# Kernel optimization log

Hardware: AMD Instinct MI355X
Metric: run time of the kernel (lower is better)

Reference implementation:

```python
import jax, jax.numpy as jnp
import numpy as np

N_NODES = 50000
N_EDGES = 400000
NODE_F = 128
EDGE_F = 64
HID = 128
N_LAYERS = 2


def _mlp(x, w1, b1, w2, b2):
    # Linear -> ReLU -> Linear
    return jnp.maximum(x @ w1 + b1, 0.0) @ w2 + b2


def setup_inputs() -> dict:
    key = jax.random.key(0)
    ks = jax.random.split(key, 24)
    s = 0.02
    inp = {
        "node_features": jax.random.normal(ks[0], (N_NODES, NODE_F), jnp.float32),
        "edge_list": jax.random.randint(ks[1], (N_EDGES, 2), 0, N_NODES, jnp.int32),
        "edge_features": jax.random.normal(ks[2], (N_EDGES, EDGE_F), jnp.float32),
        "num_nodes": N_NODES,
        # node encoder
        "ne_w1": jax.random.normal(ks[3], (NODE_F, HID), jnp.float32) * s,
        "ne_b1": jnp.zeros((HID,), jnp.float32),
        "ne_w2": jax.random.normal(ks[4], (HID, HID), jnp.float32) * s,
        "ne_b2": jnp.zeros((HID,), jnp.float32),
        # edge encoder
        "ee_w1": jax.random.normal(ks[5], (EDGE_F, HID), jnp.float32) * s,
        "ee_b1": jnp.zeros((HID,), jnp.float32),
        "ee_w2": jax.random.normal(ks[6], (HID, HID), jnp.float32) * s,
        "ee_b2": jnp.zeros((HID,), jnp.float32),
        # message layers (stacked over num_layers)
        "ml_w1": jax.random.normal(ks[7], (N_LAYERS, 3 * HID, HID), jnp.float32) * s,
        "ml_b1": jnp.zeros((N_LAYERS, HID), jnp.float32),
        "ml_w2": jax.random.normal(ks[8], (N_LAYERS, HID, HID), jnp.float32) * s,
        "ml_b2": jnp.zeros((N_LAYERS, HID), jnp.float32),
        # aggregation
        "agg_w1": jax.random.normal(ks[9], (HID, HID), jnp.float32) * s,
        "agg_b1": jnp.zeros((HID,), jnp.float32),
        "agg_w2": jax.random.normal(ks[10], (HID, HID), jnp.float32) * s,
        "agg_b2": jnp.zeros((HID,), jnp.float32),
    }
    return inp


def reference(node_features, edge_list, edge_features, num_nodes,
              ne_w1, ne_b1, ne_w2, ne_b2,
              ee_w1, ee_b1, ee_w2, ee_b2,
              ml_w1, ml_b1, ml_w2, ml_b2,
              agg_w1, agg_b1, agg_w2, agg_b2):
    node_emb = _mlp(node_features, ne_w1, ne_b1, ne_w2, ne_b2)   # [N, H]
    edge_emb = _mlp(edge_features, ee_w1, ee_b1, ee_w2, ee_b2)   # [E, H]
    src = edge_list[:, 0]
    dst = edge_list[:, 1]
    for l in range(ml_w1.shape[0]):
        h_s = node_emb[src]                                      # [E, H] gather
        h_d = node_emb[dst]                                      # [E, H] gather
        # message src->dst and dst->src (the torch loop does both directions)
        m_fwd = _mlp(jnp.concatenate([h_s, edge_emb, h_d], axis=-1),
                     ml_w1[l], ml_b1[l], ml_w2[l], ml_b2[l])     # [E, H]
        m_bwd = _mlp(jnp.concatenate([h_d, edge_emb, h_s], axis=-1),
                     ml_w1[l], ml_b1[l], ml_w2[l], ml_b2[l])     # [E, H]
        new_node_emb = node_emb.at[dst].add(m_fwd).at[src].add(m_bwd)
        node_emb = _mlp(new_node_emb, agg_w1, agg_b1, agg_w2, agg_b2)
    return node_emb
```

## Files before the change

### kernel.cpp

```cpp
#include <hip/hip_runtime.h>

typedef float fx4 __attribute__((ext_vector_type(4)));
typedef float f32x4 __attribute__((ext_vector_type(4)));
typedef unsigned short us4v __attribute__((ext_vector_type(4)));
typedef unsigned short us8 __attribute__((ext_vector_type(8)));
typedef __bf16 bf8 __attribute__((ext_vector_type(8)));

static __device__ __forceinline__ fx4 ld4(const float* p) {
    return *reinterpret_cast<const fx4*>(p);
}
static __device__ __forceinline__ void st4(float* p, fx4 v) {
    *reinterpret_cast<fx4*>(p) = v;
}
static __device__ __forceinline__ unsigned short f2bf(float f) {
    union { float f; unsigned int i; } x; x.f = f;
    unsigned int r = x.i + 0x7FFF + ((x.i >> 16) & 1);
    return (unsigned short)(r >> 16);
}
static __device__ __forceinline__ float bf2f(unsigned int u) {
    union { unsigned int i; float f; } x; x.i = u << 16; return x.f;
}
static __device__ __forceinline__ us4v pk4(f32x4 v) {
    us4v u;
    #pragma unroll
    for (int j = 0; j < 4; ++j) u[j] = f2bf(v[j]);
    return u;
}

static __device__ __forceinline__ f32x4 mfma16(us8 a, us8 b, f32x4 c) {
    return __builtin_amdgcn_mfma_f32_16x16x32_bf16(
        __builtin_bit_cast(bf8, a), __builtin_bit_cast(bf8, b), c, 0, 0, 0);
}

template <int K1, bool AF32, bool BIAS, bool RELU, bool OUTF, bool OUTB, bool XMODE>
__global__ __launch_bounds__(256) void mfma_gemm(
    const void* __restrict__ Av, const unsigned short* __restrict__ Wt,
    const float* __restrict__ bias,
    float* __restrict__ outF, unsigned short* __restrict__ outB,
    const float* __restrict__ resid, const int* __restrict__ startp, int M)
{
    constexpr int KP = K1 + 8;
    __shared__ unsigned short Ws[128 * KP];
    const int tid = threadIdx.x;
    const int lane = tid & 63;
    const int wv = tid >> 6;
    const int row0 = blockIdx.x * 128 + wv * 32;

    constexpr int C8 = K1 / 8;
    for (int i = tid; i < 128 * C8; i += 256) {
        int r = i / C8, c = (i % C8) * 8;
        *reinterpret_cast<us8*>(&Ws[r * KP + c]) =
            *reinterpret_cast<const us8*>(&Wt[r * K1 + c]);
    }
    __syncthreads();

    const int ar = lane & 15;
    const int ak = (lane >> 4) * 8;

    f32x4 acc[2][8];
    #pragma unroll
    for (int m = 0; m < 2; ++m)
        #pragma unroll
        for (int nt = 0; nt < 8; ++nt) acc[m][nt] = {0.f, 0.f, 0.f, 0.f};

    #pragma unroll
    for (int kk = 0; kk < K1 / 32; ++kk) {
        us8 a[2];
        #pragma unroll
        for (int m = 0; m < 2; ++m) {
            int row = row0 + m * 16 + ar;
            us8 t = 0;
            if (row < M) {
                if (AF32) {
                    const float* ap = (const float*)Av + (size_t)row * K1 + kk * 32 + ak;
                    fx4 x0 = ld4(ap), x1 = ld4(ap + 4);
                    #pragma unroll
                    for (int j = 0; j < 4; ++j) {
                        t[j] = f2bf(x0[j]);
                        t[4 + j] = f2bf(x1[j]);
                    }
                } else {
                    t = *reinterpret_cast<const us8*>(
                        (const unsigned short*)Av + (size_t)row * K1 + kk * 32 + ak);
                }
            }
            a[m] = t;
        }
        #pragma unroll
        for (int nt = 0; nt < 8; ++nt) {
            us8 b = *reinterpret_cast<const us8*>(&Ws[(nt * 16 + ar) * KP + kk * 32 + ak]);
            acc[0][nt] = mfma16(b, a[0], acc[0][nt]);
            acc[1][nt] = mfma16(b, a[1], acc[1][nt]);
        }
    }

    const int q = lane >> 4;
    #pragma unroll
    for (int m = 0; m < 2; ++m) {
        int r = row0 + m * 16 + (lane & 15);
        if (r >= M) continue;
        float deg = 0.f;
        if (XMODE) deg = (float)(startp[r + 1] - startp[r]);
        #pragma unroll
        for (int nt = 0; nt < 8; ++nt) {
            int c0 = nt * 16 + q * 4;
            f32x4 o = acc[m][nt];
            if (XMODE) {
                fx4 bb = ld4(bias + c0);
                fx4 rr = ld4(resid + (size_t)r * 128 + c0);
                #pragma unroll
                for (int j = 0; j < 4; ++j) o[j] += rr[j] + deg * bb[j];
            } else if (BIAS) {
                fx4 bb = ld4(bias + c0);
                #pragma unroll
                for (int j = 0; j < 4; ++j) o[j] += bb[j];
            }
            if (RELU) {
                #pragma unroll
                for (int j = 0; j < 4; ++j) o[j] = fmaxf(o[j], 0.f);
            }
            if (OUTF) st4(outF + (size_t)r * 128 + c0, o);
            if (OUTB) *reinterpret_cast<us4v*>(&outB[(size_t)r * 128 + c0]) = pk4(o);
        }
    }
}

template <bool AF32, bool OUTF, bool OUTB>
__global__ __launch_bounds__(256) void mfma_mlp(
    const void* __restrict__ Av, const unsigned short* __restrict__ W1t,
    const float* __restrict__ b1, const unsigned short* __restrict__ W2t,
    const float* __restrict__ b2,
    float* __restrict__ outF, unsigned short* __restrict__ outB, int M)
{
    constexpr int KP = 136;
    __shared__ unsigned short Ws1[128 * KP];
    __shared__ unsigned short Ws2[128 * KP];
    const int tid = threadIdx.x;
    const int lane = tid & 63;
    const int wv = tid >> 6;
    const int row0 = blockIdx.x * 128 + wv * 32;

    for (int i = tid; i < 128 * 16; i += 256) {
        int r = i >> 4, c = (i & 15) * 8;
        *reinterpret_cast<us8*>(&Ws1[r * KP + c]) =
            *reinterpret_cast<const us8*>(&W1t[r * 128 + c]);
        *reinterpret_cast<us8*>(&Ws2[r * KP + c]) =
            *reinterpret_cast<const us8*>(&W2t[r * 128 + c]);
    }
    __syncthreads();

    const int ar = lane & 15;
    const int ak = (lane >> 4) * 8;
    const int q = lane >> 4;

    f32x4 acc[2][8];
    #pragma unroll
    for (int m = 0; m < 2; ++m)
        #pragma unroll
        for (int nt = 0; nt < 8; ++nt) acc[m][nt] = {0.f, 0.f, 0.f, 0.f};

    #pragma unroll
    for (int kk = 0; kk < 4; ++kk) {
        us8 a[2];
        #pragma unroll
        for (int m = 0; m < 2; ++m) {
            int row = row0 + m * 16 + ar;
            us8 t = 0;
            if (row < M) {
                if (AF32) {
                    const float* ap = (const float*)Av + (size_t)row * 128 + kk * 32 + ak;
                    fx4 x0 = ld4(ap), x1 = ld4(ap + 4);
                    #pragma unroll
                    for (int j = 0; j < 4; ++j) {
                        t[j] = f2bf(x0[j]);
                        t[4 + j] = f2bf(x1[j]);
                    }
                } else {
                    t = *reinterpret_cast<const us8*>(
                        (const unsigned short*)Av + (size_t)row * 128 + kk * 32 + ak);
                }
            }
            a[m] = t;
        }
        #pragma unroll
        for (int nt = 0; nt < 8; ++nt) {
            us8 b = *reinterpret_cast<const us8*>(&Ws1[(nt * 16 + ar) * KP + kk * 32 + ak]);
            acc[0][nt] = mfma16(b, a[0], acc[0][nt]);
            acc[1][nt] = mfma16(b, a[1], acc[1][nt]);
        }
    }
    __syncthreads();

    #pragma unroll
    for (int m = 0; m < 2; ++m) {
        int lrow = wv * 32 + m * 16 + (lane & 15);
        #pragma unroll
        for (int nt = 0; nt < 8; ++nt) {
            int c0 = nt * 16 + q * 4;
            fx4 bb = ld4(b1 + c0);
            f32x4 o = acc[m][nt];
            #pragma unroll
            for (int j = 0; j < 4; ++j) o[j] = fmaxf(o[j] + bb[j], 0.f);
            *reinterpret_cast<us4v*>(&Ws1[lrow * KP + c0]) = pk4(o);
        }
    }
    __syncthreads();

    f32x4 acc2[2][8];
    #pragma unroll
    for (int m = 0; m < 2; ++m)
        #pragma unroll
        for (int nt = 0; nt < 8; ++nt) acc2[m][nt] = {0.f, 0.f, 0.f, 0.f};

    #pragma unroll
    for (int kk = 0; kk < 4; ++kk) {
        us8 a[2];
        #pragma unroll
        for (int m = 0; m < 2; ++m) {
            int lrow = wv * 32 + m * 16 + ar;
            a[m] = *reinterpret_cast<const us8*>(&Ws1[lrow * KP + kk * 32 + ak]);
        }
        #pragma unroll
        for (int nt = 0; nt < 8; ++nt) {
            us8 b = *reinterpret_cast<const us8*>(&Ws2[(nt * 16 + ar) * KP + kk * 32 + ak]);
            acc2[0][nt] = mfma16(b, a[0], acc2[0][nt]);
            acc2[1][nt] = mfma16(b, a[1], acc2[1][nt]);
        }
    }

    #pragma unroll
    for (int m = 0; m < 2; ++m) {
        int r = row0 + m * 16 + (lane & 15);
        if (r >= M) continue;
        #pragma unroll
        for (int nt = 0; nt < 8; ++nt) {
            int c0 = nt * 16 + q * 4;
            fx4 bb = ld4(b2 + c0);
            f32x4 o = acc2[m][nt];
            #pragma unroll
            for (int j = 0; j < 4; ++j) o[j] += bb[j];
            if (OUTF) st4(outF + (size_t)r * 128 + c0, o);
            if (OUTB) *reinterpret_cast<us4v*>(&outB[(size_t)r * 128 + c0]) = pk4(o);
        }
    }
}

__global__ __launch_bounds__(256) void mfma_gemm_dual(
    const float* __restrict__ A, const unsigned short* __restrict__ Wt,
    unsigned short* __restrict__ out1, unsigned short* __restrict__ out2, int M)
{
    constexpr int KP = 136;
    __shared__ unsigned short Ws[256 * KP];
    const int tid = threadIdx.x;
    const int lane = tid & 63;
    const int wv = tid >> 6;
    const int row0 = blockIdx.x * 128 + wv * 32;

    for (int i = tid; i < 256 * 16; i += 256) {
        int r = i >> 4, c = (i & 15) * 8;
        *reinterpret_cast<us8*>(&Ws[r * KP + c]) =
            *reinterpret_cast<const us8*>(&Wt[r * 128 + c]);
    }
    __syncthreads();

    const int ar = lane & 15;
    const int ak = (lane >> 4) * 8;
    const int q = lane >> 4;

    f32x4 acc[2][16];
    #pragma unroll
    for (int m = 0; m < 2; ++m)
        #pragma unroll
        for (int nt = 0; nt < 16; ++nt) acc[m][nt] = {0.f, 0.f, 0.f, 0.f};

    #pragma unroll
    for (int kk = 0; kk < 4; ++kk) {
        us8 a[2];
        #pragma unroll
        for (int m = 0; m < 2; ++m) {
            int row = row0 + m * 16 + ar;
            us8 t = 0;
            if (row < M) {
                const float* ap = A + (size_t)row * 128 + kk * 32 + ak;
                fx4 x0 = ld4(ap), x1 = ld4(ap + 4);
                #pragma unroll
                for (int j = 0; j < 4; ++j) {
                    t[j] = f2bf(x0[j]);
                    t[4 + j] = f2bf(x1[j]);
                }
            }
            a[m] = t;
        }
        #pragma unroll
        for (int nt = 0; nt < 16; ++nt) {
            us8 b = *reinterpret_cast<const us8*>(&Ws[(nt * 16 + ar) * KP + kk * 32 + ak]);
            acc[0][nt] = mfma16(b, a[0], acc[0][nt]);
            acc[1][nt] = mfma16(b, a[1], acc[1][nt]);
        }
    }

    #pragma unroll
    for (int m = 0; m < 2; ++m) {
        int r = row0 + m * 16 + (lane & 15);
        if (r >= M) continue;
        #pragma unroll
        for (int nt = 0; nt < 16; ++nt) {
            int c0 = (nt & 7) * 16 + q * 4;
            unsigned short* o = (nt < 8) ? out1 : out2;
            *reinterpret_cast<us4v*>(&o[(size_t)r * 128 + c0]) = pk4(acc[m][nt]);
        }
    }
}

__global__ __launch_bounds__(256) void gemm128_kernel(
    const float* __restrict__ X, const float* __restrict__ W,
    float* __restrict__ Out, int M)
{
    __shared__ float Xs[64 * 132];
    const int tid = threadIdx.x;
    const int row0 = blockIdx.x * 64;

    for (int i = tid; i < 64 * 32; i += 256) {
        int r = i >> 5, c = (i & 31) * 4;
        fx4 v = {0.f, 0.f, 0.f, 0.f};
        int gr = row0 + r;
        if (gr < M) v = ld4(X + (size_t)gr * 128 + c);
        st4(&Xs[r * 132 + c], v);
    }
    __syncthreads();

    const int ty = tid >> 4, tx = tid & 15;
    fx4 acc[4][2];
    #pragma unroll
    for (int r = 0; r < 4; ++r) { acc[r][0] = 0.f; acc[r][1] = 0.f; }
    for (int k = 0; k < 128; k += 4) {
        fx4 xr[4];
        #pragma unroll
        for (int r = 0; r < 4; ++r) xr[r] = ld4(&Xs[(ty * 4 + r) * 132 + k]);
        #pragma unroll
        for (int kk = 0; kk < 4; ++kk) {
            fx4 wa = ld4(W + (size_t)(k + kk) * 128 + tx * 8);
            fx4 wb = ld4(W + (size_t)(k + kk) * 128 + tx * 8 + 4);
            #pragma unroll
            for (int r = 0; r < 4; ++r) {
                acc[r][0] += xr[r][kk] * wa;
                acc[r][1] += xr[r][kk] * wb;
            }
        }
    }
    #pragma unroll
    for (int r = 0; r < 4; ++r) {
        int gr = row0 + ty * 4 + r;
        if (gr < M) {
            st4(Out + (size_t)gr * 128 + tx * 8, acc[r][0]);
            st4(Out + (size_t)gr * 128 + tx * 8 + 4, acc[r][1]);
        }
    }
}

struct TJob { const float* src; unsigned short* dst; int K; };
struct TJobs { TJob j[16]; };

__global__ __launch_bounds__(256) void transpose_kernel(TJobs jobs) {
    TJob t = jobs.j[blockIdx.x];
    int total = 128 * t.K;
    for (int i = threadIdx.x; i < total; i += 256) {
        int n = i / t.K, k = i - n * t.K;
        t.dst[(size_t)n * t.K + k] = f2bf(t.src[(size_t)k * 128 + n]);
    }
}

__global__ __launch_bounds__(128) void bep_kernel(
    const float* __restrict__ ee_b2, const float* __restrict__ ml_w1,
    const float* __restrict__ ml_b1, float* __restrict__ bep)
{
    int l = blockIdx.x, n = threadIdx.x;
    const float* W1b = ml_w1 + (size_t)l * 384 * 128 + 128 * 128;
    float s = ml_b1[(size_t)l * 128 + n];
    for (int k = 0; k < 128; ++k) s += ee_b2[k] * W1b[(size_t)k * 128 + n];
    bep[(size_t)l * 128 + n] = s;
}

__global__ __launch_bounds__(256) void csr_hist_kernel(
    const int* __restrict__ el, int* __restrict__ cnt, int NE)
{
    int e = blockIdx.x * 256 + threadIdx.x;
    if (e < NE) {
        atomicAdd(&cnt[el[2 * (size_t)e + 1]], 1);
        atomicAdd(&cnt[el[2 * (size_t)e]], 1);
    }
}

__global__ __launch_bounds__(256) void scan_p1_kernel(
    const int* __restrict__ cnt, int* __restrict__ bsum, int NN)
{
    __shared__ int red[256];
    const int t = threadIdx.x;
    int i = blockIdx.x * 256 + t;
    red[t] = (i < NN) ? cnt[i] : 0;
    __syncthreads();
    for (int off = 128; off > 0; off >>= 1) {
        if (t < off) red[t] += red[t + off];
        __syncthreads();
    }
    if (t == 0) bsum[blockIdx.x] = red[0];
}

__global__ __launch_bounds__(256) void scan_p2_kernel(
    int* __restrict__ bsum, int* __restrict__ startp, int nb, int NN)
{
    __shared__ int part[256];
    const int t = threadIdx.x;
    int v = (t < nb) ? bsum[t] : 0;
    part[t] = v;
    __syncthreads();
    for (int off = 1; off < 256; off <<= 1) {
        int u = (t >= off) ? part[t - off] : 0;
        __syncthreads();
        part[t] += u;
        __syncthreads();
    }
    if (t < nb) bsum[t] = part[t] - v;
    if (t == 255) startp[NN] = part[255];
}

__global__ __launch_bounds__(256) void scan_p3_kernel(
    int* __restrict__ cnt, const int* __restrict__ bsum,
    int* __restrict__ startp, int NN)
{
    __shared__ int part[256];
    const int t = threadIdx.x;
    int i = blockIdx.x * 256 + t;
    int v = (i < NN) ? cnt[i] : 0;
    part[t] = v;
    __syncthreads();
    for (int off = 1; off < 256; off <<= 1) {
        int u = (t >= off) ? part[t - off] : 0;
        __syncthreads();
        part[t] += u;
        __syncthreads();
    }
    if (i < NN) {
        startp[i] = bsum[blockIdx.x] + part[t] - v;
        cnt[i] = 0;
    }
}

__global__ __launch_bounds__(256) void csr_fill_kernel(
    const int* __restrict__ el, const int* __restrict__ startp,
    int* __restrict__ cursor, int2* __restrict__ inc, int NE)
{
    int e = blockIdx.x * 256 + threadIdx.x;
    if (e < NE) {
        int s = el[2 * (size_t)e], d = el[2 * (size_t)e + 1];
        int p = startp[d] + atomicAdd(&cursor[d], 1);
        inc[p] = make_int2(s, e);
        int q = startp[s] + atomicAdd(&cursor[s], 1);
        inc[q] = make_int2(d, e);
    }
}

__global__ __launch_bounds__(256) void gather_kernel(
    const unsigned short* __restrict__ P1bf, const unsigned short* __restrict__ P3bf,
    const unsigned short* __restrict__ Ep, const int2* __restrict__ inc,
    const int* __restrict__ startp, unsigned short* __restrict__ S, int M)
{
    const int tid = threadIdx.x;
    const int lane = tid & 63;
    const int n = blockIdx.x * 4 + (tid >> 6);
    if (n >= M) return;
    const int slot = lane >> 4;
    const int c = (lane & 15) * 8;

    float p3[8], acc[8];
    us8 u3 = *reinterpret_cast<const us8*>(&P3bf[(size_t)n * 128 + c]);
    #pragma unroll
    for (int i = 0; i < 8; ++i) {
        p3[i] = bf2f((unsigned int)(unsigned short)u3[i]);
        acc[i] = 0.f;
    }

    const int j1 = startp[n + 1];
    int j = startp[n] + slot;
    int2 oe = (j < j1) ? inc[j] : make_int2(0, 0);
    while (j < j1) {
        int jn = j + 4;
        int2 oen = (jn < j1) ? inc[jn] : make_int2(0, 0);
        us8 u1 = *reinterpret_cast<const us8*>(&P1bf[(size_t)oe.x * 128 + c]);
        us8 ue = *reinterpret_cast<const us8*>(&Ep[(size_t)oe.y * 128 + c]);
        #pragma unroll
        for (int i = 0; i < 8; ++i)
            acc[i] += fmaxf(p3[i] + bf2f((unsigned int)(unsigned short)u1[i])
                                  + bf2f((unsigned int)(unsigned short)ue[i]), 0.f);
        j = jn; oe = oen;
    }

    #pragma unroll
    for (int i = 0; i < 8; ++i) {
        acc[i] += __shfl_xor(acc[i], 16, 64);
        acc[i] += __shfl_xor(acc[i], 32, 64);
    }
    if (slot == 0) {
        us8 pk;
        #pragma unroll
        for (int i = 0; i < 8; ++i) pk[i] = f2bf(acc[i]);
        *reinterpret_cast<us8*>(&S[(size_t)n * 128 + c]) = pk;
    }
}

extern "C" void kernel_launch(void* const* d_in, const int* in_sizes, int n_in,
                              void* d_out, int out_size, void* d_ws, size_t ws_size,
                              hipStream_t stream) {
    const float* node_f    = (const float*)d_in[0];
    const int*   edge_list = (const int*)d_in[1];
    const float* edge_f    = (const float*)d_in[2];
    const float* ne_w1 = (const float*)d_in[4];
    const float* ne_b1 = (const float*)d_in[5];
    const float* ne_w2 = (const float*)d_in[6];
    const float* ne_b2 = (const float*)d_in[7];
    const float* ee_w1 = (const float*)d_in[8];
    const float* ee_b1 = (const float*)d_in[9];
    const float* ee_w2 = (const float*)d_in[10];
    const float* ee_b2 = (const float*)d_in[11];
    const float* ml_w1 = (const float*)d_in[12];
    const float* ml_b1 = (const float*)d_in[13];
    const float* ml_w2 = (const float*)d_in[14];
    const float* ml_b2 = (const float*)d_in[15];
    const float* agg_w1 = (const float*)d_in[16];
    const float* agg_b1 = (const float*)d_in[17];
    const float* agg_w2 = (const float*)d_in[18];
    const float* agg_b2 = (const float*)d_in[19];

    const int NN = in_sizes[0] / 128;
    const int NE = in_sizes[1] / 2;
    const int n_layers = in_sizes[12] / (384 * 128);

    char* p = (char*)d_ws;
    auto alloc = [&](size_t bytes) -> void* {
        void* r = (void*)p;
        p += (bytes + 255) & ~(size_t)255;
        return r;
    };
    float* node_emb = (float*)alloc((size_t)NN * 128 * 4);
    unsigned short* P1bf = (unsigned short*)alloc((size_t)NN * 128 * 2);
    unsigned short* P3bf = (unsigned short*)alloc((size_t)NN * 128 * 2);
    unsigned short* bufS = (unsigned short*)alloc((size_t)NN * 128 * 2);
    unsigned short* H_edge = (unsigned short*)alloc((size_t)NE * 128 * 2);
    unsigned short* Ep = (unsigned short*)alloc((size_t)NE * 128 * 2);
    unsigned short* ne_w1t = (unsigned short*)alloc(128 * 128 * 2);
    unsigned short* ne_w2t = (unsigned short*)alloc(128 * 128 * 2);
    unsigned short* ee_w1t = (unsigned short*)alloc(128 * 64 * 2);
    unsigned short* aw1t = (unsigned short*)alloc(128 * 128 * 2);
    unsigned short* aw2t = (unsigned short*)alloc(128 * 128 * 2);
    unsigned short* W13t[2], *W2t[2], *Wept[2];
    float* Wepf[2];
    for (int l = 0; l < 2; ++l) {
        W13t[l] = (unsigned short*)alloc(256 * 128 * 2);
        W2t[l]  = (unsigned short*)alloc(128 * 128 * 2);
        Wept[l] = (unsigned short*)alloc(128 * 128 * 2);
        Wepf[l] = (float*)alloc(128 * 128 * 4);
    }
    float* bep = (float*)alloc((size_t)2 * 128 * 4);
    int* cnt = (int*)alloc((size_t)NN * 4);
    int* startp = (int*)alloc((size_t)(NN + 1) * 4);
    int* bsum = (int*)alloc(256 * 4);
    int2* inc = (int2*)alloc((size_t)2 * NE * 8);
    size_t need = (size_t)(p - (char*)d_ws);
    if (ws_size < need) return;

    dim3 blk(256);
    const int gM_N = (NN + 127) / 128;
    const int gM_E = (NE + 127) / 128;
    const int gE256 = (NE + 255) / 256;
    const int nbScan = (NN + 255) / 256;

    for (int l = 0; l < n_layers && l < 2; ++l) {
        const float* W1b = ml_w1 + (size_t)l * 384 * 128 + 128 * 128;
        gemm128_kernel<<<2, blk, 0, stream>>>(ee_w2, W1b, Wepf[l], 128);
    }
    {
        TJobs jobs{};
        int nj = 0;
        jobs.j[nj++] = {ne_w1, ne_w1t, 128};
        jobs.j[nj++] = {ne_w2, ne_w2t, 128};
        jobs.j[nj++] = {ee_w1, ee_w1t, 64};
        jobs.j[nj++] = {agg_w1, aw1t, 128};
        jobs.j[nj++] = {agg_w2, aw2t, 128};
        for (int l = 0; l < n_layers && l < 2; ++l) {
            jobs.j[nj++] = {ml_w1 + (size_t)l * 384 * 128, W13t[l], 128};
            jobs.j[nj++] = {ml_w1 + (size_t)l * 384 * 128 + 256 * 128, W13t[l] + 128 * 128, 128};
            jobs.j[nj++] = {ml_w2 + (size_t)l * 128 * 128, W2t[l], 128};
            jobs.j[nj++] = {Wepf[l], Wept[l], 128};
        }
        transpose_kernel<<<nj, blk, 0, stream>>>(jobs);
    }
    bep_kernel<<<n_layers, 128, 0, stream>>>(ee_b2, ml_w1, ml_b1, bep);

    mfma_mlp<true, true, false><<<gM_N, blk, 0, stream>>>(
        node_f, ne_w1t, ne_b1, ne_w2t, ne_b2, node_emb, nullptr, NN);
    mfma_gemm<64, true, true, true, false, true, false><<<gM_E, blk, 0, stream>>>(
        edge_f, ee_w1t, ee_b1, nullptr, H_edge, nullptr, nullptr, NE);

    hipMemsetAsync(cnt, 0, (size_t)NN * sizeof(int), stream);
    csr_hist_kernel<<<gE256, blk, 0, stream>>>(edge_list, cnt, NE);
    scan_p1_kernel<<<nbScan, blk, 0, stream>>>(cnt, bsum, NN);
    scan_p2_kernel<<<1, blk, 0, stream>>>(bsum, startp, nbScan, NN);
    scan_p3_kernel<<<nbScan, blk, 0, stream>>>(cnt, bsum, startp, NN);
    csr_fill_kernel<<<gE256, blk, 0, stream>>>(edge_list, startp, cnt, inc, NE);

    float* out = (float*)d_out;
    for (int l = 0; l < n_layers && l < 2; ++l) {
        mfma_gemm_dual<<<gM_N, blk, 0, stream>>>(node_emb, W13t[l], P1bf, P3bf, NN);
        mfma_gemm<128, false, true, false, false, true, false><<<gM_E, blk, 0, stream>>>(
            H_edge, Wept[l], bep + (size_t)l * 128, nullptr, Ep, nullptr, nullptr, NE);
        gather_kernel<<<(NN + 3) / 4, blk, 0, stream>>>(
            P1bf, P3bf, Ep, inc, startp, bufS, NN);
        mfma_gemm<128, false, true, false, false, true, true><<<gM_N, blk, 0, stream>>>(
            bufS, W2t[l], ml_b2 + (size_t)l * 128, nullptr, P1bf, node_emb, startp, NN);
        float* dst = (l == n_layers - 1) ? out : node_emb;
        mfma_mlp<false, true, false><<<gM_N, blk, 0, stream>>>(
            P1bf, aw1t, agg_b1, aw2t, agg_b2, dst, nullptr, NN);
    }
}
```

Measured before the change: 588.0 us.

## Fuse edge encoder with per-layer edge projections and read weights from global

Adds an edge_mega kernel that computes the edge encoder hidden layer into LDS and then directly produces both layers' projected edge terms. This removes the H_edge intermediate round trip and the per-layer edge GEMM launches. The GEMM and MLP kernels also stop staging weights in LDS and load B fragments straight from global or L2, which cuts LDS use and the startup sync but adds repeated global loads. The dual node GEMM is split into two single GEMMs, which reads node_emb twice.

```diff
diff --git a/kernel.cpp b/kernel.cpp
--- a/kernel.cpp
+++ b/kernel.cpp
@@ -30,6 +30,29 @@
 static __device__ __forceinline__ f32x4 mfma16(us8 a, us8 b, f32x4 c) {
     return __builtin_amdgcn_mfma_f32_16x16x32_bf16(
         __builtin_bit_cast(bf8, a), __builtin_bit_cast(bf8, b), c, 0, 0, 0);
+}
+
+template <int K1, bool AF32>
+static __device__ __forceinline__ void loadA(
+    const void* __restrict__ Av, int row0, int ar, int ak, int kk, int M, us8 a[2])
+{
+    #pragma unroll
+    for (int m = 0; m < 2; ++m) {
+        int row = row0 + m * 16 + ar;
+        us8 t = 0;
+        if (row < M) {
+            if (AF32) {
+                const float* ap = (const float*)Av + (size_t)row * K1 + kk * 32 + ak;
+                fx4 x0 = ld4(ap), x1 = ld4(ap + 4);
+                #pragma unroll
+                for (int j = 0; j < 4; ++j) { t[j] = f2bf(x0[j]); t[4 + j] = f2bf(x1[j]); }
+            } else {
+                t = *reinterpret_cast<const us8*>(
+                    (const unsigned short*)Av + (size_t)row * K1 + kk * 32 + ak);
+            }
+        }
+        a[m] = t;
+    }
 }
 
 template <int K1, bool AF32, bool BIAS, bool RELU, bool OUTF, bool OUTB, bool XMODE>
@@ -39,21 +62,11 @@
     float* __restrict__ outF, unsigned short* __restrict__ outB,
     const float* __restrict__ resid, const int* __restrict__ startp, int M)
 {
-    constexpr int KP = K1 + 8;
-    __shared__ unsigned short Ws[128 * KP];
     const int tid = threadIdx.x;
     const int lane = tid & 63;
     const int wv = tid >> 6;
     const int row0 = blockIdx.x * 128 + wv * 32;
 
-    constexpr int C8 = K1 / 8;
-    for (int i = tid; i < 128 * C8; i += 256) {
-        int r = i / C8, c = (i % C8) * 8;
-        *reinterpret_cast<us8*>(&Ws[r * KP + c]) =
-            *reinterpret_cast<const us8*>(&Wt[r * K1 + c]);
-    }
-    __syncthreads();
-
     const int ar = lane & 15;
     const int ak = (lane >> 4) * 8;
 
@@ -66,31 +79,16 @@
     #pragma unroll
     for (int kk = 0; kk < K1 / 32; ++kk) {
         us8 a[2];
-        #pragma unroll
-        for (int m = 0; m < 2; ++m) {
-            int row = row0 + m * 16 + ar;
-            us8 t = 0;
-            if (row < M) {
-                if (AF32) {
-                    const float* ap = (const float*)Av + (size_t)row * K1 + kk * 32 + ak;
-                    fx4 x0 = ld4(ap), x1 = ld4(ap + 4);
-                    #pragma unroll
-                    for (int j = 0; j < 4; ++j) {
-                        t[j] = f2bf(x0[j]);
-                        t[4 + j] = f2bf(x1[j]);
-                    }
-                } else {
-                    t = *reinterpret_cast<const us8*>(
-                        (const unsigned short*)Av + (size_t)row * K1 + kk * 32 + ak);
-                }
-            }
-            a[m] = t;
-        }
-        #pragma unroll
-        for (int nt = 0; nt < 8; ++nt) {
-            us8 b = *reinterpret_cast<const us8*>(&Ws[(nt * 16 + ar) * KP + kk * 32 + ak]);
-            acc[0][nt] = mfma16(b, a[0], acc[0][nt]);
-            acc[1][nt] = mfma16(b, a[1], acc[1][nt]);
+        loadA<K1, AF32>(Av, row0, ar, ak, kk, M, a);
+        us8 b[8];
+        #pragma unroll
+        for (int nt = 0; nt < 8; ++nt)
+            b[nt] = *reinterpret_cast<const us8*>(
+                &Wt[(size_t)(nt * 16 + ar) * K1 + kk * 32 + ak]);
+        #pragma unroll
+        for (int nt = 0; nt < 8; ++nt) {
+            acc[0][nt] = mfma16(b[nt], a[0], acc[0][nt]);
+            acc[1][nt] = mfma16(b[nt], a[1], acc[1][nt]);
         }
     }
 
@@ -133,22 +131,12 @@
     float* __restrict__ outF, unsigned short* __restrict__ outB, int M)
 {
     constexpr int KP = 136;
-    __shared__ unsigned short Ws1[128 * KP];
-    __shared__ unsigned short Ws2[128 * KP];
+    __shared__ unsigned short Hs[128 * KP];
     const int tid = threadIdx.x;
     const int lane = tid & 63;
     const int wv = tid >> 6;
     const int row0 = blockIdx.x * 128 + wv * 32;
 
-    for (int i = tid; i < 128 * 16; i += 256) {
-        int r = i >> 4, c = (i & 15) * 8;
-        *reinterpret_cast<us8*>(&Ws1[r * KP + c]) =
-            *reinterpret_cast<const us8*>(&W1t[r * 128 + c]);
-        *reinterpret_cast<us8*>(&Ws2[r * KP + c]) =
-            *reinterpret_cast<const us8*>(&W2t[r * 128 + c]);
-    }
-    __syncthreads();
-
     const int ar = lane & 15;
     const int ak = (lane >> 4) * 8;
     const int q = lane >> 4;
@@ -162,34 +150,18 @@
     #pragma unroll
     for (int kk = 0; kk < 4; ++kk) {
         us8 a[2];
-        #pragma unroll
-        for (int m = 0; m < 2; ++m) {
-            int row = row0 + m * 16 + ar;
-            us8 t = 0;
-            if (row < M) {
-                if (AF32) {
-                    const float* ap = (const float*)Av + (size_t)row * 128 + kk * 32 + ak;
-                    fx4 x0 = ld4(ap), x1 = ld4(ap + 4);
-                    #pragma unroll
-                    for (int j = 0; j < 4; ++j) {
-                        t[j] = f2bf(x0[j]);
-                        t[4 + j] = f2bf(x1[j]);
-                    }
-                } else {
-                    t = *reinterpret_cast<const us8*>(
-                        (const unsigned short*)Av + (size_t)row * 128 + kk * 32 + ak);
-                }
-            }
-            a[m] = t;
-        }
-        #pragma unroll
-        for (int nt = 0; nt < 8; ++nt) {
-            us8 b = *reinterpret_cast<const us8*>(&Ws1[(nt * 16 + ar) * KP + kk * 32 + ak]);
-            acc[0][nt] = mfma16(b, a[0], acc[0][nt]);
-            acc[1][nt] = mfma16(b, a[1], acc[1][nt]);
-        }
-    }
-    __syncthreads();
+        loadA<128, AF32>(Av, row0, ar, ak, kk, M, a);
+        us8 b[8];
+        #pragma unroll
+        for (int nt = 0; nt < 8; ++nt)
+            b[nt] = *reinterpret_cast<const us8*>(
+                &W1t[(size_t)(nt * 16 + ar) * 128 + kk * 32 + ak]);
+        #pragma unroll
+        for (int nt = 0; nt < 8; ++nt) {
+            acc[0][nt] = mfma16(b[nt], a[0], acc[0][nt]);
+            acc[1][nt] = mfma16(b[nt], a[1], acc[1][nt]);
+        }
+    }
 
     #pragma unroll
     for (int m = 0; m < 2; ++m) {
@@ -201,7 +173,7 @@
             f32x4 o = acc[m][nt];
             #pragma unroll
             for (int j = 0; j < 4; ++j) o[j] = fmaxf(o[j] + bb[j], 0.f);
-            *reinterpret_cast<us4v*>(&Ws1[lrow * KP + c0]) = pk4(o);
+            *reinterpret_cast<us4v*>(&Hs[lrow * KP + c0]) = pk4(o);
         }
     }
     __syncthreads();
@@ -216,15 +188,18 @@
     for (int kk = 0; kk < 4; ++kk) {
         us8 a[2];
         #pragma unroll
-        for (int m = 0; m < 2; ++m) {
-            int lrow = wv * 32 + m * 16 + ar;
-            a[m] = *reinterpret_cast<const us8*>(&Ws1[lrow * KP + kk * 32 + ak]);
-        }
-        #pragma unroll
-        for (int nt = 0; nt < 8; ++nt) {
-            us8 b = *reinterpret_cast<const us8*>(&Ws2[(nt * 16 + ar) * KP + kk * 32 + ak]);
-            acc2[0][nt] = mfma16(b, a[0], acc2[0][nt]);
-            acc2[1][nt] = mfma16(b, a[1], acc2[1][nt]);
+        for (int m = 0; m < 2; ++m)
+            a[m] = *reinterpret_cast<const us8*>(
+                &Hs[(wv * 32 + m * 16 + ar) * KP + kk * 32 + ak]);
+        us8 b[8];
+        #pragma unroll
+        for (int nt = 0; nt < 8; ++nt)
+            b[nt] = *reinterpret_cast<const us8*>(
+                &W2t[(size_t)(nt * 16 + ar) * 128 + kk * 32 + ak]);
+        #pragma unroll
+        for (int nt = 0; nt < 8; ++nt) {
+            acc2[0][nt] = mfma16(b[nt], a[0], acc2[0][nt]);
+            acc2[1][nt] = mfma16(b[nt], a[1], acc2[1][nt]);
         }
     }
 
@@ -245,69 +220,105 @@
     }
 }
 
-__global__ __launch_bounds__(256) void mfma_gemm_dual(
-    const float* __restrict__ A, const unsigned short* __restrict__ Wt,
-    unsigned short* __restrict__ out1, unsigned short* __restrict__ out2, int M)
+__global__ __launch_bounds__(256) void edge_mega(
+    const float* __restrict__ edge_f, const unsigned short* __restrict__ W1t,
+    const float* __restrict__ b1,
+    const unsigned short* __restrict__ Wep0t, const unsigned short* __restrict__ Wep1t,
+    const float* __restrict__ bep,
+    unsigned short* __restrict__ Ep0, unsigned short* __restrict__ Ep1,
+    int nout, int M)
 {
     constexpr int KP = 136;
-    __shared__ unsigned short Ws[256 * KP];
+    __shared__ unsigned short Hs[128 * KP];
     const int tid = threadIdx.x;
     const int lane = tid & 63;
     const int wv = tid >> 6;
     const int row0 = blockIdx.x * 128 + wv * 32;
 
-    for (int i = tid; i < 256 * 16; i += 256) {
-        int r = i >> 4, c = (i & 15) * 8;
-        *reinterpret_cast<us8*>(&Ws[r * KP + c]) =
-            *reinterpret_cast<const us8*>(&Wt[r * 128 + c]);
-    }
-    __syncthreads();
-
     const int ar = lane & 15;
     const int ak = (lane >> 4) * 8;
     const int q = lane >> 4;
 
-    f32x4 acc[2][16];
+    f32x4 acc[2][8];
     #pragma unroll
     for (int m = 0; m < 2; ++m)
         #pragma unroll
-        for (int nt = 0; nt < 16; ++nt) acc[m][nt] = {0.f, 0.f, 0.f, 0.f};
-
-    #pragma unroll
-    for (int kk = 0; kk < 4; ++kk) {
+        for (int nt = 0; nt < 8; ++nt) acc[m][nt] = {0.f, 0.f, 0.f, 0.f};
+
+    #pragma unroll
+    for (int kk = 0; kk < 2; ++kk) {
         us8 a[2];
+        loadA<64, true>(edge_f, row0, ar, ak, kk, M, a);
+        us8 b[8];
+        #pragma unroll
+        for (int nt = 0; nt < 8; ++nt)
+            b[nt] = *reinterpret_cast<const us8*>(
+                &W1t[(size_t)(nt * 16 + ar) * 64 + kk * 32 + ak]);
+        #pragma unroll
+        for (int nt = 0; nt < 8; ++nt) {
+            acc[0][nt] = mfma16(b[nt], a[0], acc[0][nt]);
+            acc[1][nt] = mfma16(b[nt], a[1], acc[1][nt]);
+        }
+    }
+
+    #pragma unroll
+    for (int m = 0; m < 2; ++m) {
+        int lrow = wv * 32 + m * 16 + (lane & 15);
+        #pragma unroll
+        for (int nt = 0; nt < 8; ++nt) {
+            int c0 = nt * 16 + q * 4;
+            fx4 bb = ld4(b1 + c0);
+            f32x4 o = acc[m][nt];
+            #pragma unroll
+            for (int j = 0; j < 4; ++j) o[j] = fmaxf(o[j] + bb[j], 0.f);
+            *reinterpret_cast<us4v*>(&Hs[lrow * KP + c0]) = pk4(o);
+        }
+    }
+    __syncthreads();
+
+    for (int l = 0; l < nout; ++l) {
+        const unsigned short* Wt = (l == 0) ? Wep0t : Wep1t;
+        unsigned short* Out = (l == 0) ? Ep0 : Ep1;
+        const float* bl = bep + (size_t)l * 128;
+
+        f32x4 acc2[2][8];
+        #pragma unroll
+        for (int m = 0; m < 2; ++m)
+            #pragma unroll
+            for (int nt = 0; nt < 8; ++nt) acc2[m][nt] = {0.f, 0.f, 0.f, 0.f};
+
+        #pragma unroll
+        for (int kk = 0; kk < 4; ++kk) {
+            us8 a[2];
+            #pragma unroll
+            for (int m = 0; m < 2; ++m)
+                a[m] = *reinterpret_cast<const us8*>(
+                    &Hs[(wv * 32 + m * 16 + ar) * KP + kk * 32 + ak]);
+            us8 b[8];
+            #pragma unroll
+            for (int nt = 0; nt < 8; ++nt)
+                b[nt] = *reinterpret_cast<const us8*>(
+                    &Wt[(size_t)(nt * 16 + ar) * 128 + kk * 32 + ak]);
+            #pragma unroll
+            for (int nt = 0; nt < 8; ++nt) {
+                acc2[0][nt] = mfma16(b[nt], a[0], acc2[0][nt]);
+                acc2[1][nt] = mfma16(b[nt], a[1], acc2[1][nt]);
+            }
+        }
+
         #pragma unroll
         for (int m = 0; m < 2; ++m) {
-            int row = row0 + m * 16 + ar;
-            us8 t = 0;
-            if (row < M) {
-                const float* ap = A + (size_t)row * 128 + kk * 32 + ak;
-                fx4 x0 = ld4(ap), x1 = ld4(ap + 4);
+            int r = row0 + m * 16 + (lane & 15);
+            if (r >= M) continue;
+            #pragma unroll
+            for (int nt = 0; nt < 8; ++nt) {
+                int c0 = nt * 16 + q * 4;
+                fx4 bb = ld4(bl + c0);
+                f32x4 o = acc2[m][nt];
                 #pragma unroll
-                for (int j = 0; j < 4; ++j) {
-                    t[j] = f2bf(x0[j]);
-                    t[4 + j] = f2bf(x1[j]);
-                }
+                for (int j = 0; j < 4; ++j) o[j] += bb[j];
+                *reinterpret_cast<us4v*>(&Out[(size_t)r * 128 + c0]) = pk4(o);
             }
-            a[m] = t;
-        }
-        #pragma unroll
-        for (int nt = 0; nt < 16; ++nt) {
-            us8 b = *reinterpret_cast<const us8*>(&Ws[(nt * 16 + ar) * KP + kk * 32 + ak]);
-            acc[0][nt] = mfma16(b, a[0], acc[0][nt]);
-            acc[1][nt] = mfma16(b, a[1], acc[1][nt]);
-        }
-    }
-
-    #pragma unroll
-    for (int m = 0; m < 2; ++m) {
-        int r = row0 + m * 16 + (lane & 15);
-        if (r >= M) continue;
-        #pragma unroll
-        for (int nt = 0; nt < 16; ++nt) {
-            int c0 = (nt & 7) * 16 + q * 4;
-            unsigned short* o = (nt < 8) ? out1 : out2;
-            *reinterpret_cast<us4v*>(&o[(size_t)r * 128 + c0]) = pk4(acc[m][nt]);
         }
     }
 }
@@ -545,8 +556,8 @@
     unsigned short* P1bf = (unsigned short*)alloc((size_t)NN * 128 * 2);
     unsigned short* P3bf = (unsigned short*)alloc((size_t)NN * 128 * 2);
     unsigned short* bufS = (unsigned short*)alloc((size_t)NN * 128 * 2);
-    unsigned short* H_edge = (unsigned short*)alloc((size_t)NE * 128 * 2);
-    unsigned short* Ep = (unsigned short*)alloc((size_t)NE * 128 * 2);
+    unsigned short* Ep0 = (unsigned short*)alloc((size_t)NE * 128 * 2);
+    unsigned short* Ep1 = (unsigned short*)alloc((size_t)NE * 128 * 2);
     unsigned short* ne_w1t = (unsigned short*)alloc(128 * 128 * 2);
     unsigned short* ne_w2t = (unsigned short*)alloc(128 * 128 * 2);
     unsigned short* ee_w1t = (unsigned short*)alloc(128 * 64 * 2);
@@ -598,8 +609,9 @@
 
     mfma_mlp<true, true, false><<<gM_N, blk, 0, stream>>>(
         node_f, ne_w1t, ne_b1, ne_w2t, ne_b2, node_emb, nullptr, NN);
-    mfma_gemm<64, true, true, true, false, true, false><<<gM_E, blk, 0, stream>>>(
-        edge_f, ee_w1t, ee_b1, nullptr, H_edge, nullptr, nullptr, NE);
+    edge_mega<<<gM_E, blk, 0, stream>>>(
+        edge_f, ee_w1t, ee_b1, Wept[0], Wept[n_layers > 1 ? 1 : 0], bep,
+        Ep0, Ep1, (n_layers > 1) ? 2 : 1, NE);
 
     hipMemsetAsync(cnt, 0, (size_t)NN * sizeof(int), stream);
     csr_hist_kernel<<<gE256, blk, 0, stream>>>(edge_list, cnt, NE);
@@ -610,11 +622,12 @@
 
     float* out = (float*)d_out;
     for (int l = 0; l < n_layers && l < 2; ++l) {
-        mfma_gemm_dual<<<gM_N, blk, 0, stream>>>(node_emb, W13t[l], P1bf, P3bf, NN);
-        mfma_gemm<128, false, true, false, false, true, false><<<gM_E, blk, 0, stream>>>(
-            H_edge, Wept[l], bep + (size_t)l * 128, nullptr, Ep, nullptr, nullptr, NE);
+        mfma_gemm<128, true, false, false, false, true, false><<<gM_N, blk, 0, stream>>>(
+            node_emb, W13t[l], nullptr, nullptr, P1bf, nullptr, nullptr, NN);
+        mfma_gemm<128, true, false, false, false, true, false><<<gM_N, blk, 0, stream>>>(
+            node_emb, W13t[l] + 128 * 128, nullptr, nullptr, P3bf, nullptr, nullptr, NN);
         gather_kernel<<<(NN + 3) / 4, blk, 0, stream>>>(
-            P1bf, P3bf, Ep, inc, startp, bufS, NN);
+            P1bf, P3bf, (l == 0) ? Ep0 : Ep1, inc, startp, bufS, NN);
         mfma_gemm<128, false, true, false, false, true, true><<<gM_N, blk, 0, stream>>>(
             bufS, W2t[l], ml_b2 + (size_t)l * 128, nullptr, P1bf, node_emb, startp, NN);
         float* dst = (l == n_layers - 1) ? out : node_emb;
```

After: 669.6 us. 1.14x slower.
